# Kernel optimization log

Measured on AMD Instinct MI355X. Metric: run time of the kernel, lower is better.

## Reference

```python
import jax, jax.numpy as jnp
import numpy as np

PADDING = 300
NMS_THRESH = 0.5


def bbox_transform_inv(boxes, deltas):
    # boxes: (N,4) x1,y1,x2,y2 ; deltas: (N,4*C) -> (N,4*C) decoded boxes
    w = boxes[:, 2] - boxes[:, 0] + 1.0
    h = boxes[:, 3] - boxes[:, 1] + 1.0
    cx = boxes[:, 0] + 0.5 * w
    cy = boxes[:, 1] + 0.5 * h
    dx, dy = deltas[:, 0::4], deltas[:, 1::4]
    dw, dh = deltas[:, 2::4], deltas[:, 3::4]
    pcx = dx * w[:, None] + cx[:, None]
    pcy = dy * h[:, None] + cy[:, None]
    pw = jnp.exp(dw) * w[:, None]
    ph = jnp.exp(dh) * h[:, None]
    out = jnp.stack([pcx - 0.5 * pw, pcy - 0.5 * ph,
                     pcx + 0.5 * pw, pcy + 0.5 * ph], axis=2)  # (N,C,4)
    return out.reshape(boxes.shape[0], -1)


def clip_boxes(boxes, hw):
    # hw = (H, W); boxes (N, 4*C)
    b = boxes.reshape(boxes.shape[0], -1, 4)
    x1 = jnp.clip(b[..., 0], 0.0, hw[1] - 1.0)
    y1 = jnp.clip(b[..., 1], 0.0, hw[0] - 1.0)
    x2 = jnp.clip(b[..., 2], 0.0, hw[1] - 1.0)
    y2 = jnp.clip(b[..., 3], 0.0, hw[0] - 1.0)
    return jnp.stack([x1, y1, x2, y2], axis=2).reshape(boxes.shape[0], -1)


def nms(boxes, scores, max_out, thresh):
    # Greedy NMS: sequential argmax + IoU suppression (fixed max_out iters).
    N = boxes.shape[0]
    x1, y1, x2, y2 = boxes[:, 0], boxes[:, 1], boxes[:, 2], boxes[:, 3]
    areas = (x2 - x1 + 1.0) * (y2 - y1 + 1.0)
    neg_inf = jnp.array(-jnp.inf, boxes.dtype)

    def step(s, _):
        i = jnp.argmax(s)
        valid = s[i] > neg_inf
        xx1 = jnp.maximum(x1[i], x1)
        yy1 = jnp.maximum(y1[i], y1)
        xx2 = jnp.minimum(x2[i], x2)
        yy2 = jnp.minimum(y2[i], y2)
        inter = jnp.maximum(xx2 - xx1 + 1.0, 0.0) * jnp.maximum(yy2 - yy1 + 1.0, 0.0)
        iou = inter / (areas[i] + areas - inter)
        suppress = (iou > thresh) | (jnp.arange(N) == i)
        s = jnp.where(suppress, neg_inf, s)
        return s, (i, valid)

    _, (idx, valid) = jax.lax.scan(step, scores, None, length=max_out)
    return idx, valid


def reference(metadata, deltas, proposals, scores, masks):
    N = proposals.shape[1]
    C = scores.shape[2]
    prop = proposals.reshape(-1, 4)
    boxes = prop / metadata[0, 2]                       # undo image scale
    d = deltas.reshape(N, -1)
    pred = bbox_transform_inv(boxes, d)                 # (N, 4C)
    pred = clip_boxes(pred, metadata[0, :2])
    sc = scores.reshape(N, C)
    top = jnp.argmax(sc, axis=1)                        # most probable class
    predc = pred.reshape(N, C, 4)
    pbox = jnp.take_along_axis(predc, top[:, None, None], axis=1)[:, 0, :]  # (N,4)
    max_scores = jnp.max(sc[:, 1:], axis=1)             # skip background col
    idx, valid = nms(jax.lax.stop_gradient(pbox),
                     jax.lax.stop_gradient(max_scores), PADDING, NMS_THRESH)
    vf = valid.astype(pbox.dtype)
    out_boxes = pbox[idx] * vf[:, None]                 # (300,4), zero padded
    out_scores = sc[idx] * vf[:, None]                  # (300,C)
    out_masks = masks[0][idx] * vf[:, None, None, None] # (300,mh,mw,mc)
    return out_boxes[None], out_scores[None], out_masks[None]


def setup_inputs() -> dict:
    key = jax.random.key(0)
    k1, k2, k3, k4, k5 = jax.random.split(key, 5)
    N, C, MH, MW, MC = 6000, 81, 14, 14, 81
    H, W, SCALE = 600.0, 800.0, 1.6
    metadata = jnp.array([[H, W, SCALE]], dtype=jnp.float32)
    # proposals: valid boxes inside the scaled image
    xy = jax.random.uniform(k1, (N, 2), jnp.float32) * jnp.array([W - 120.0, H - 120.0], jnp.float32)
    wh = jax.random.uniform(k2, (N, 2), jnp.float32) * 100.0 + 16.0
    proposals = jnp.concatenate([xy, xy + wh], axis=1)[None] * SCALE  # (1,N,4)
    deltas = jax.random.normal(k3, (1, N, 4 * C), jnp.float32) * 0.1
    scores = jax.random.uniform(k4, (1, N, C), jnp.float32)
    masks = jax.random.uniform(k5, (1, N, MH, MW, MC), jnp.float32)
    return {"metadata": metadata, "deltas": deltas, "proposals": proposals,
            "scores": scores, "masks": masks}
```

## Files before the change

### kernel.cpp

```cpp
#include <hip/hip_runtime.h>
#include <math.h>

#pragma STDC FP_CONTRACT OFF

#define N 6000
#define NPAD 6144
#define C 81
#define PADDING 300
#define NMS_THRESH 0.5f
#define MASK_ELEMS (14 * 14 * 81)
#define MASK_W 96
#define NCHUNK 8
#define CHUNK 750
#define LOOK 8

typedef unsigned long long u64;

__global__ void decode_kernel(const float* __restrict__ meta,
                              const float* __restrict__ deltas,
                              const float* __restrict__ proposals,
                              const float* __restrict__ scores,
                              float* __restrict__ pbox,
                              float* __restrict__ area,
                              u64* __restrict__ skey) {
    int n = blockIdx.x * blockDim.x + threadIdx.x;
    if (n >= N) return;

    float Hm = meta[0], Wm = meta[1], scale = meta[2];

    float b0 = proposals[n * 4 + 0] / scale;
    float b1 = proposals[n * 4 + 1] / scale;
    float b2 = proposals[n * 4 + 2] / scale;
    float b3 = proposals[n * 4 + 3] / scale;
    float w = b2 - b0 + 1.0f;
    float h = b3 - b1 + 1.0f;
    float cx = b0 + 0.5f * w;
    float cy = b1 + 0.5f * h;

    const float* sr = scores + n * C;
    int top = 0;
    float best = sr[0];
    float ms = -INFINITY;
    for (int c = 1; c < C; ++c) {
        float s = sr[c];
        if (s > best) { best = s; top = c; }
        ms = fmaxf(ms, s);
    }

    const float* dr = deltas + n * (4 * C) + 4 * top;
    float dx = dr[0], dy = dr[1], dw = dr[2], dh = dr[3];
    float pcx = dx * w + cx;
    float pcy = dy * h + cy;
    float pw = expf(dw) * w;
    float ph = expf(dh) * h;
    float x1 = pcx - 0.5f * pw;
    float y1 = pcy - 0.5f * ph;
    float x2 = pcx + 0.5f * pw;
    float y2 = pcy + 0.5f * ph;
    x1 = fminf(fmaxf(x1, 0.0f), Wm - 1.0f);
    y1 = fminf(fmaxf(y1, 0.0f), Hm - 1.0f);
    x2 = fminf(fmaxf(x2, 0.0f), Wm - 1.0f);
    y2 = fminf(fmaxf(y2, 0.0f), Hm - 1.0f);

    pbox[n * 4 + 0] = x1;
    pbox[n * 4 + 1] = y1;
    pbox[n * 4 + 2] = x2;
    pbox[n * 4 + 3] = y2;
    area[n] = (x2 - x1 + 1.0f) * (y2 - y1 + 1.0f);

    unsigned int b = __float_as_uint(ms);
    unsigned int u = b ^ ((b & 0x80000000u) ? 0xFFFFFFFFu : 0x80000000u);
    skey[n] = ((u64)u << 32) | (unsigned int)(~n);
}

__global__ void rank_kernel(const u64* __restrict__ skey,
                            int* __restrict__ rank_part) {
    __shared__ u64 lk[CHUNK];
    int chunk = blockIdx.y;
    int t = threadIdx.x;
    int j0 = chunk * CHUNK;
    for (int j = t; j < CHUNK; j += 256) lk[j] = skey[j0 + j];
    __syncthreads();

    int i = blockIdx.x * 256 + t;
    if (i >= N) return;
    u64 mykey = skey[i];
    int cnt = 0;
    for (int j = 0; j < CHUNK; ++j) cnt += (lk[j] > mykey) ? 1 : 0;
    rank_part[chunk * NPAD + i] = cnt;
}

__global__ void scatter_kernel(const int* __restrict__ rank_part,
                               const float* __restrict__ pbox,
                               const float* __restrict__ area,
                               int* __restrict__ sidx,
                               float* __restrict__ sx1, float* __restrict__ sy1,
                               float* __restrict__ sx2, float* __restrict__ sy2,
                               float* __restrict__ sarea) {
    int i = blockIdx.x * blockDim.x + threadIdx.x;
    if (i >= N) return;
    int r = 0;
    for (int c = 0; c < NCHUNK; ++c) r += rank_part[c * NPAD + i];
    sidx[r] = i;
    sx1[r] = pbox[i * 4 + 0];
    sy1[r] = pbox[i * 4 + 1];
    sx2[r] = pbox[i * 4 + 2];
    sy2[r] = pbox[i * 4 + 3];
    sarea[r] = area[i];
}

__global__ void __launch_bounds__(256) iou_kernel(const float* __restrict__ sx1,
                                                  const float* __restrict__ sy1,
                                                  const float* __restrict__ sx2,
                                                  const float* __restrict__ sy2,
                                                  const float* __restrict__ sarea,
                                                  u64* __restrict__ mask) {
    int p = blockIdx.x * 4 + (threadIdx.x >> 6);
    int lane = threadIdx.x & 63;
    if (p >= N) return;

    float wx1 = sx1[p], wy1 = sy1[p], wx2 = sx2[p], wy2 = sy2[p];
    float war = sarea[p];
    u64* row = mask + (size_t)p * MASK_W;

    for (int w = 0; w < 94; ++w) {
        int q = w * 64 + lane;
        float xx1 = fmaxf(wx1, sx1[q]);
        float yy1 = fmaxf(wy1, sy1[q]);
        float xx2 = fminf(wx2, sx2[q]);
        float yy2 = fminf(wy2, sy2[q]);
        float inter = fmaxf(xx2 - xx1 + 1.0f, 0.0f) * fmaxf(yy2 - yy1 + 1.0f, 0.0f);
        float iou = inter / (war + sarea[q] - inter);
        u64 bal = __ballot(iou > NMS_THRESH);
        if (lane == 0) row[w] = bal;
    }
}

__global__ void scan_kernel(const u64* __restrict__ mask,
                            const int* __restrict__ sidx,
                            int* __restrict__ out_idx,
                            float* __restrict__ out_valid) {
    int lane = threadIdx.x;
    int w0 = 2 * lane, w1 = 2 * lane + 1;

    u64 m_lo = (w0 < 93) ? 0ULL : (w0 == 93 ? 0xFFFF000000000000ULL : ~0ULL);
    u64 m_hi = (w1 < 93) ? 0ULL : (w1 == 93 ? 0xFFFF000000000000ULL : ~0ULL);

    u64 cx[LOOK], cy[LOOK];
#pragma unroll
    for (int k = 0; k < LOOK; ++k) { cx[k] = 0; cy[k] = 0; }
    int base = -1000000;

    int r = 0;
    while (r < PADDING) {
        u64 z0 = ~m_lo, z1 = ~m_hi;
        u64 bal = __ballot((z0 | z1) != 0ULL);
        if (bal == 0ULL) break;
        int lsrc = (int)__ffsll(bal) - 1;
        int local = (z0 != 0ULL) ? ((int)__ffsll(z0) - 1) : (64 + (int)__ffsll(z1) - 1);
        int p = __shfl(lane * 128 + local, lsrc);

        if (p > base + (LOOK - 1)) {
            base = p;
            if (lane < 48) {
#pragma unroll
                for (int k = 0; k < LOOK; ++k) {
                    int rowp = min(p + k, N - 1);
                    const u64* rp = mask + (size_t)rowp * MASK_W + 2 * lane;
                    cx[k] = rp[0];
                    cy[k] = rp[1];
                }
            }
        }
        int s = p - base;
        u64 vx = cx[0], vy = cy[0];
#pragma unroll
        for (int k = 1; k < LOOK; ++k) {
            if (s == k) { vx = cx[k]; vy = cy[k]; }
        }
        if (lane < 48) { m_lo |= vx; m_hi |= vy; }
        if (lane == 0) { out_idx[r] = sidx[p]; out_valid[r] = 1.0f; }
        ++r;
    }
    for (; r < PADDING; ++r) {
        if (lane == 0) { out_idx[r] = 0; out_valid[r] = 0.0f; }
    }
}

__global__ void gather_kernel(const float* __restrict__ pbox,
                              const float* __restrict__ scores,
                              const float* __restrict__ masks,
                              const int* __restrict__ idx,
                              const float* __restrict__ valid,
                              float* __restrict__ out) {
    int b = blockIdx.x;
    int tid = threadIdx.x;
    int i = idx[b];
    float vf = valid[b];

    if (tid < 4) out[b * 4 + tid] = pbox[i * 4 + tid] * vf;
    if (tid < C) out[PADDING * 4 + b * C + tid] = scores[i * C + tid] * vf;

    const float4* src = (const float4*)(masks + (size_t)i * MASK_ELEMS);
    float4* dst = (float4*)(out + PADDING * 4 + PADDING * C + (size_t)b * MASK_ELEMS);
    for (int m = tid; m < MASK_ELEMS / 4; m += 256) {
        float4 v = src[m];
        dst[m] = make_float4(v.x * vf, v.y * vf, v.z * vf, v.w * vf);
    }
}

extern "C" void kernel_launch(void* const* d_in, const int* in_sizes, int n_in,
                              void* d_out, int out_size, void* d_ws, size_t ws_size,
                              hipStream_t stream) {
    const float* meta      = (const float*)d_in[0];
    const float* deltas    = (const float*)d_in[1];
    const float* proposals = (const float*)d_in[2];
    const float* scores    = (const float*)d_in[3];
    const float* masks     = (const float*)d_in[4];
    float* out = (float*)d_out;

    char* ws = (char*)d_ws;
    u64*   mask      = (u64*)(ws);
    u64*   skey      = (u64*)(ws + 4608000);
    float* pbox      = (float*)(ws + 4657152);
    float* area      = (float*)(ws + 4753152);
    int*   rank_part = (int*)(ws + 4777152);
    int*   sidx      = (int*)(ws + 4973760);
    float* sx1       = (float*)(ws + 4998336);
    float* sy1       = (float*)(ws + 5022912);
    float* sx2       = (float*)(ws + 5047488);
    float* sy2       = (float*)(ws + 5072064);
    float* sarea     = (float*)(ws + 5096640);
    int*   out_idx   = (int*)(ws + 5121216);
    float* out_valid = (float*)(ws + 5122416);

    decode_kernel<<<24, 256, 0, stream>>>(meta, deltas, proposals, scores, pbox, area, skey);
    rank_kernel<<<dim3(24, NCHUNK), 256, 0, stream>>>(skey, rank_part);
    scatter_kernel<<<24, 256, 0, stream>>>(rank_part, pbox, area, sidx, sx1, sy1, sx2, sy2, sarea);
    iou_kernel<<<1500, 256, 0, stream>>>(sx1, sy1, sx2, sy2, sarea, mask);
    scan_kernel<<<1, 64, 0, stream>>>(mask, sidx, out_idx, out_valid);
    gather_kernel<<<PADDING, 256, 0, stream>>>(pbox, scores, masks, out_idx, out_valid, out);
}
```

Measured before the change: 612.1 us.

## Parallelize decode per warp, compute upper-triangle IoU, double-bank scan prefetch, split gather

The decode kernel now assigns one 64-lane wavefront per proposal and finds the top class and max score with a shuffle reduction, replacing the serial per-thread loop over 81 scores. Sorted boxes are stored as float4, and the IoU kernel computes only the upper-triangular words, with each wave handling a row pair (g, N-1-g) to balance work; areas are recomputed on the fly. The single-wave scan replaces its sliding lookahead window with two alternating 8-row banks, prefetching the next block so that reloads happen less often. The gather kernel is split into 4 parts per output row to expose more parallelism. These changes add complexity, and the scan relies on lower-triangle mask words never being read.

```diff
diff --git a/kernel.cpp b/kernel.cpp
--- a/kernel.cpp
+++ b/kernel.cpp
@@ -12,7 +12,6 @@
 #define MASK_W 96
 #define NCHUNK 8
 #define CHUNK 750
-#define LOOK 8
 
 typedef unsigned long long u64;
 
@@ -21,56 +20,59 @@
                               const float* __restrict__ proposals,
                               const float* __restrict__ scores,
                               float* __restrict__ pbox,
-                              float* __restrict__ area,
                               u64* __restrict__ skey) {
-    int n = blockIdx.x * blockDim.x + threadIdx.x;
-    if (n >= N) return;
-
-    float Hm = meta[0], Wm = meta[1], scale = meta[2];
-
-    float b0 = proposals[n * 4 + 0] / scale;
-    float b1 = proposals[n * 4 + 1] / scale;
-    float b2 = proposals[n * 4 + 2] / scale;
-    float b3 = proposals[n * 4 + 3] / scale;
-    float w = b2 - b0 + 1.0f;
-    float h = b3 - b1 + 1.0f;
-    float cx = b0 + 0.5f * w;
-    float cy = b1 + 0.5f * h;
-
-    const float* sr = scores + n * C;
-    int top = 0;
-    float best = sr[0];
-    float ms = -INFINITY;
-    for (int c = 1; c < C; ++c) {
-        float s = sr[c];
-        if (s > best) { best = s; top = c; }
-        ms = fmaxf(ms, s);
-    }
-
-    const float* dr = deltas + n * (4 * C) + 4 * top;
-    float dx = dr[0], dy = dr[1], dw = dr[2], dh = dr[3];
-    float pcx = dx * w + cx;
-    float pcy = dy * h + cy;
-    float pw = expf(dw) * w;
-    float ph = expf(dh) * h;
-    float x1 = pcx - 0.5f * pw;
-    float y1 = pcy - 0.5f * ph;
-    float x2 = pcx + 0.5f * pw;
-    float y2 = pcy + 0.5f * ph;
-    x1 = fminf(fmaxf(x1, 0.0f), Wm - 1.0f);
-    y1 = fminf(fmaxf(y1, 0.0f), Hm - 1.0f);
-    x2 = fminf(fmaxf(x2, 0.0f), Wm - 1.0f);
-    y2 = fminf(fmaxf(y2, 0.0f), Hm - 1.0f);
-
-    pbox[n * 4 + 0] = x1;
-    pbox[n * 4 + 1] = y1;
-    pbox[n * 4 + 2] = x2;
-    pbox[n * 4 + 3] = y2;
-    area[n] = (x2 - x1 + 1.0f) * (y2 - y1 + 1.0f);
-
-    unsigned int b = __float_as_uint(ms);
-    unsigned int u = b ^ ((b & 0x80000000u) ? 0xFFFFFFFFu : 0x80000000u);
-    skey[n] = ((u64)u << 32) | (unsigned int)(~n);
+    int gw = blockIdx.x * 4 + (threadIdx.x >> 6);
+    int lane = threadIdx.x & 63;
+    if (gw >= N) return;
+
+    const float* sr = scores + gw * C;
+    float s0 = (lane < C) ? sr[lane] : -INFINITY;
+    float s1 = (lane + 64 < C) ? sr[lane + 64] : -INFINITY;
+
+    float bs;
+    int bc;
+    if (s1 > s0) { bs = s1; bc = lane + 64; } else { bs = s0; bc = lane; }
+    float ms = fmaxf((lane == 0) ? -INFINITY : s0, s1);
+
+    for (int off = 32; off > 0; off >>= 1) {
+        float os = __shfl_down(bs, off);
+        int oc = __shfl_down(bc, off);
+        if (os > bs || (os == bs && oc < bc)) { bs = os; bc = oc; }
+        ms = fmaxf(ms, __shfl_down(ms, off));
+    }
+
+    if (lane == 0) {
+        float Hm = meta[0], Wm = meta[1], scale = meta[2];
+        float4 pr = *(const float4*)(proposals + gw * 4);
+        float b0 = pr.x / scale;
+        float b1 = pr.y / scale;
+        float b2 = pr.z / scale;
+        float b3 = pr.w / scale;
+        float w = b2 - b0 + 1.0f;
+        float h = b3 - b1 + 1.0f;
+        float cx = b0 + 0.5f * w;
+        float cy = b1 + 0.5f * h;
+
+        float4 dl = *(const float4*)(deltas + (size_t)gw * (4 * C) + 4 * bc);
+        float pcx = dl.x * w + cx;
+        float pcy = dl.y * h + cy;
+        float pw = expf(dl.z) * w;
+        float ph = expf(dl.w) * h;
+        float x1 = pcx - 0.5f * pw;
+        float y1 = pcy - 0.5f * ph;
+        float x2 = pcx + 0.5f * pw;
+        float y2 = pcy + 0.5f * ph;
+        x1 = fminf(fmaxf(x1, 0.0f), Wm - 1.0f);
+        y1 = fminf(fmaxf(y1, 0.0f), Hm - 1.0f);
+        x2 = fminf(fmaxf(x2, 0.0f), Wm - 1.0f);
+        y2 = fminf(fmaxf(y2, 0.0f), Hm - 1.0f);
+
+        *(float4*)(pbox + gw * 4) = make_float4(x1, y1, x2, y2);
+
+        unsigned int b = __float_as_uint(ms);
+        unsigned int u = b ^ ((b & 0x80000000u) ? 0xFFFFFFFFu : 0x80000000u);
+        skey[gw] = ((u64)u << 32) | (unsigned int)(~gw);
+    }
 }
 
 __global__ void rank_kernel(const u64* __restrict__ skey,
@@ -92,64 +94,73 @@
 
 __global__ void scatter_kernel(const int* __restrict__ rank_part,
                                const float* __restrict__ pbox,
-                               const float* __restrict__ area,
                                int* __restrict__ sidx,
-                               float* __restrict__ sx1, float* __restrict__ sy1,
-                               float* __restrict__ sx2, float* __restrict__ sy2,
-                               float* __restrict__ sarea) {
+                               float4* __restrict__ sbox) {
     int i = blockIdx.x * blockDim.x + threadIdx.x;
     if (i >= N) return;
     int r = 0;
     for (int c = 0; c < NCHUNK; ++c) r += rank_part[c * NPAD + i];
     sidx[r] = i;
-    sx1[r] = pbox[i * 4 + 0];
-    sy1[r] = pbox[i * 4 + 1];
-    sx2[r] = pbox[i * 4 + 2];
-    sy2[r] = pbox[i * 4 + 3];
-    sarea[r] = area[i];
-}
-
-__global__ void __launch_bounds__(256) iou_kernel(const float* __restrict__ sx1,
-                                                  const float* __restrict__ sy1,
-                                                  const float* __restrict__ sx2,
-                                                  const float* __restrict__ sy2,
-                                                  const float* __restrict__ sarea,
+    sbox[r] = *(const float4*)(pbox + i * 4);
+}
+
+__global__ void __launch_bounds__(256) iou_kernel(const float4* __restrict__ sbox,
                                                   u64* __restrict__ mask) {
-    int p = blockIdx.x * 4 + (threadIdx.x >> 6);
+    int g = blockIdx.x * 4 + (threadIdx.x >> 6);
     int lane = threadIdx.x & 63;
-    if (p >= N) return;
-
-    float wx1 = sx1[p], wy1 = sy1[p], wx2 = sx2[p], wy2 = sy2[p];
-    float war = sarea[p];
-    u64* row = mask + (size_t)p * MASK_W;
-
-    for (int w = 0; w < 94; ++w) {
-        int q = w * 64 + lane;
-        float xx1 = fmaxf(wx1, sx1[q]);
-        float yy1 = fmaxf(wy1, sy1[q]);
-        float xx2 = fminf(wx2, sx2[q]);
-        float yy2 = fminf(wy2, sy2[q]);
-        float inter = fmaxf(xx2 - xx1 + 1.0f, 0.0f) * fmaxf(yy2 - yy1 + 1.0f, 0.0f);
-        float iou = inter / (war + sarea[q] - inter);
-        u64 bal = __ballot(iou > NMS_THRESH);
-        if (lane == 0) row[w] = bal;
-    }
-}
+    if (g >= 3000) return;
+
+#pragma unroll
+    for (int which = 0; which < 2; ++which) {
+        int p = which ? (N - 1 - g) : g;
+        float4 B = sbox[p];
+        float war = (B.z - B.x + 1.0f) * (B.w - B.y + 1.0f);
+        u64* row = mask + (size_t)p * MASK_W;
+        for (int w = (p >> 6); w < 94; ++w) {
+            int q = (w << 6) + lane;
+            float4 Q = sbox[q];
+            float qa = (Q.z - Q.x + 1.0f) * (Q.w - Q.y + 1.0f);
+            float xx1 = fmaxf(B.x, Q.x);
+            float yy1 = fmaxf(B.y, Q.y);
+            float xx2 = fminf(B.z, Q.z);
+            float yy2 = fminf(B.w, Q.w);
+            float inter = fmaxf(xx2 - xx1 + 1.0f, 0.0f) * fmaxf(yy2 - yy1 + 1.0f, 0.0f);
+            float iou = inter / (war + qa - inter);
+            u64 bal = __ballot(iou > NMS_THRESH);
+            if (lane == 0) row[w] = bal;
+        }
+    }
+}
+
+#define LOADBANK(X, Y, BIDX)                                              \
+    do {                                                                  \
+        const u64* _rp = mask + (size_t)(BIDX) * 8 * MASK_W + w0;         \
+        _Pragma("unroll") for (int _k = 0; _k < 8; ++_k) {                \
+            X[_k] = _rp[0];                                               \
+            Y[_k] = _rp[1];                                               \
+            _rp += MASK_W;                                                \
+        }                                                                 \
+    } while (0)
 
 __global__ void scan_kernel(const u64* __restrict__ mask,
                             const int* __restrict__ sidx,
                             int* __restrict__ out_idx,
                             float* __restrict__ out_valid) {
     int lane = threadIdx.x;
-    int w0 = 2 * lane, w1 = 2 * lane + 1;
+    int w0 = 2 * lane, w1 = w0 + 1;
 
     u64 m_lo = (w0 < 93) ? 0ULL : (w0 == 93 ? 0xFFFF000000000000ULL : ~0ULL);
     u64 m_hi = (w1 < 93) ? 0ULL : (w1 == 93 ? 0xFFFF000000000000ULL : ~0ULL);
 
-    u64 cx[LOOK], cy[LOOK];
-#pragma unroll
-    for (int k = 0; k < LOOK; ++k) { cx[k] = 0; cy[k] = 0; }
-    int base = -1000000;
+    u64 ax[8], ay[8], bx[8], by[8];
+#pragma unroll
+    for (int k = 0; k < 8; ++k) { ax[k] = 0; ay[k] = 0; bx[k] = 0; by[k] = 0; }
+
+    int curBlk = 0;
+    if (lane < 48) {
+        LOADBANK(ax, ay, 0);
+        LOADBANK(bx, by, 1);
+    }
 
     int r = 0;
     while (r < PADDING) {
@@ -160,23 +171,38 @@
         int local = (z0 != 0ULL) ? ((int)__ffsll(z0) - 1) : (64 + (int)__ffsll(z1) - 1);
         int p = __shfl(lane * 128 + local, lsrc);
 
-        if (p > base + (LOOK - 1)) {
-            base = p;
+        int blk = p >> 3;
+        if (blk >= curBlk + 2) {
             if (lane < 48) {
-#pragma unroll
-                for (int k = 0; k < LOOK; ++k) {
-                    int rowp = min(p + k, N - 1);
-                    const u64* rp = mask + (size_t)rowp * MASK_W + 2 * lane;
-                    cx[k] = rp[0];
-                    cy[k] = rp[1];
+                if ((blk & 1) == 0) {
+                    LOADBANK(ax, ay, blk);
+                    LOADBANK(bx, by, blk + 1);
+                } else {
+                    LOADBANK(bx, by, blk);
+                    LOADBANK(ax, ay, blk + 1);
                 }
             }
+            curBlk = blk;
+        } else if (blk == curBlk + 1) {
+            if (lane < 48) {
+                if ((curBlk & 1) == 0) LOADBANK(ax, ay, curBlk + 2);
+                else                   LOADBANK(bx, by, curBlk + 2);
+            }
+            curBlk = blk;
         }
-        int s = p - base;
-        u64 vx = cx[0], vy = cy[0];
-#pragma unroll
-        for (int k = 1; k < LOOK; ++k) {
-            if (s == k) { vx = cx[k]; vy = cy[k]; }
+
+        int sel = p & 7;
+        u64 vx, vy;
+        if ((blk & 1) == 0) {
+            vx = ax[0]; vy = ay[0];
+#pragma unroll
+            for (int k = 1; k < 8; ++k)
+                if (sel == k) { vx = ax[k]; vy = ay[k]; }
+        } else {
+            vx = bx[0]; vy = by[0];
+#pragma unroll
+            for (int k = 1; k < 8; ++k)
+                if (sel == k) { vx = bx[k]; vy = by[k]; }
         }
         if (lane < 48) { m_lo |= vx; m_hi |= vy; }
         if (lane == 0) { out_idx[r] = sidx[p]; out_valid[r] = 1.0f; }
@@ -194,16 +220,20 @@
                               const float* __restrict__ valid,
                               float* __restrict__ out) {
     int b = blockIdx.x;
+    int part = blockIdx.y;
     int tid = threadIdx.x;
     int i = idx[b];
     float vf = valid[b];
 
-    if (tid < 4) out[b * 4 + tid] = pbox[i * 4 + tid] * vf;
-    if (tid < C) out[PADDING * 4 + b * C + tid] = scores[i * C + tid] * vf;
+    if (part == 0) {
+        if (tid < 4) out[b * 4 + tid] = pbox[i * 4 + tid] * vf;
+        if (tid < C) out[PADDING * 4 + b * C + tid] = scores[i * C + tid] * vf;
+    }
 
     const float4* src = (const float4*)(masks + (size_t)i * MASK_ELEMS);
     float4* dst = (float4*)(out + PADDING * 4 + PADDING * C + (size_t)b * MASK_ELEMS);
-    for (int m = tid; m < MASK_ELEMS / 4; m += 256) {
+    int end = min((part + 1) * 993, MASK_ELEMS / 4);
+    for (int m = part * 993 + tid; m < end; m += 256) {
         float4 v = src[m];
         dst[m] = make_float4(v.x * vf, v.y * vf, v.z * vf, v.w * vf);
     }
@@ -220,24 +250,19 @@
     float* out = (float*)d_out;
 
     char* ws = (char*)d_ws;
-    u64*   mask      = (u64*)(ws);
-    u64*   skey      = (u64*)(ws + 4608000);
-    float* pbox      = (float*)(ws + 4657152);
-    float* area      = (float*)(ws + 4753152);
-    int*   rank_part = (int*)(ws + 4777152);
-    int*   sidx      = (int*)(ws + 4973760);
-    float* sx1       = (float*)(ws + 4998336);
-    float* sy1       = (float*)(ws + 5022912);
-    float* sx2       = (float*)(ws + 5047488);
-    float* sy2       = (float*)(ws + 5072064);
-    float* sarea     = (float*)(ws + 5096640);
-    int*   out_idx   = (int*)(ws + 5121216);
-    float* out_valid = (float*)(ws + 5122416);
-
-    decode_kernel<<<24, 256, 0, stream>>>(meta, deltas, proposals, scores, pbox, area, skey);
+    u64*    mask      = (u64*)(ws);
+    u64*    skey      = (u64*)(ws + 4608000);
+    float*  pbox      = (float*)(ws + 4657152);
+    int*    rank_part = (int*)(ws + 4753152);
+    int*    sidx      = (int*)(ws + 4949760);
+    float4* sbox      = (float4*)(ws + 4974336);
+    int*    out_idx   = (int*)(ws + 5072640);
+    float*  out_valid = (float*)(ws + 5073840);
+
+    decode_kernel<<<1500, 256, 0, stream>>>(meta, deltas, proposals, scores, pbox, skey);
     rank_kernel<<<dim3(24, NCHUNK), 256, 0, stream>>>(skey, rank_part);
-    scatter_kernel<<<24, 256, 0, stream>>>(rank_part, pbox, area, sidx, sx1, sy1, sx2, sy2, sarea);
-    iou_kernel<<<1500, 256, 0, stream>>>(sx1, sy1, sx2, sy2, sarea, mask);
+    scatter_kernel<<<24, 256, 0, stream>>>(rank_part, pbox, sidx, sbox);
+    iou_kernel<<<752, 256, 0, stream>>>(sbox, mask);
     scan_kernel<<<1, 64, 0, stream>>>(mask, sidx, out_idx, out_valid);
-    gather_kernel<<<PADDING, 256, 0, stream>>>(pbox, scores, masks, out_idx, out_valid, out);
-}
+    gather_kernel<<<dim3(PADDING, 4), 256, 0, stream>>>(pbox, scores, masks, out_idx, out_valid, out);
+}
```

After: 620.9 us. Within noise of the previous version (+1.4%).
